# Performance work log

Measured on AMD Instinct MI355X. Metric: run time of the kernel, lower is better.

The kernel has to match this reference:

```python
import jax, jax.numpy as jnp
import numpy as np

B, T, Hs, Ws, D, NH, NKV = 2, 8, 16, 16, 1024, 16, 4
HD = D // NH  # 64
EPS = 1e-6
THETA = 10000.0


def setup_inputs() -> dict:
    key = jax.random.key(0)
    ks = jax.random.split(key, 6)
    N = T * Hs * Ws
    s = 0.02
    return {
        'x': jax.random.normal(ks[0], (B, N, D), jnp.float32),
        'Wq': jax.random.normal(ks[1], (D, D), jnp.float32) * s,
        'bq': jnp.zeros((D,), jnp.float32),
        'Wk': jax.random.normal(ks[2], (D, NKV * HD), jnp.float32) * s,
        'bk': jnp.zeros((NKV * HD,), jnp.float32),
        'Wv': jax.random.normal(ks[3], (D, NKV * HD), jnp.float32) * s,
        'bv': jnp.zeros((NKV * HD,), jnp.float32),
        'Wo': jax.random.normal(ks[4], (D, D), jnp.float32) * s,
        'bo': jnp.zeros((D,), jnp.float32),
        'qn_w': jnp.ones((HD,), jnp.float32),
        'kn_w': jnp.ones((HD,), jnp.float32),
        't': T, 'h': Hs, 'w': Ws,
    }


def _rms_norm(x, w):
    # RMSNorm over last dim (head_dim), eps=1e-6, learned scale
    var = jnp.mean(jnp.square(x), axis=-1, keepdims=True)
    return x * jax.lax.rsqrt(var + EPS) * w


def _rope_cs(n, d):
    inv = 1.0 / (THETA ** (np.arange(0, d, 2, dtype=np.float32) / d))
    fr = np.arange(n, dtype=np.float32)[:, None] * inv[None, :]
    emb = np.concatenate([fr, fr], axis=-1)  # (n, d)
    return jnp.asarray(np.cos(emb)), jnp.asarray(np.sin(emb))


def _rot_half(x):
    x1, x2 = jnp.split(x, 2, axis=-1)
    return jnp.concatenate([-x2, x1], axis=-1)


def _st_rope(x, t, h, w):
    # x: (B, t, h, w, heads, hd); factored 3D RoPE on head_dim split
    d = x.shape[-1]
    if d % 3 == 0:
        dt = dh = d // 3
        dw = d - 2 * dt
    else:
        dt = d // 4
        dh = d // 4
        dw = d - dt - dh
    xt, xh, xw = jnp.split(x, [dt, dt + dh], axis=-1)

    def app(xs, n, axis_pos, dd):
        cos, sin = _rope_cs(n, dd)
        shp = [1] * 6
        shp[axis_pos] = n
        shp[-1] = dd
        cos = cos.reshape(shp)
        sin = sin.reshape(shp)
        return xs * cos + _rot_half(xs) * sin

    xt = app(xt, t, 1, dt)
    xh = app(xh, h, 2, dh)
    xw = app(xw, w, 3, dw)
    return jnp.concatenate([xt, xh, xw], axis=-1)


def reference(x, Wq, bq, Wk, bk, Wv, bv, Wo, bo, qn_w, kn_w, t, h, w):
    Bx, N, Dx = x.shape
    q = (x @ Wq + bq).reshape(Bx, N, NH, HD)
    k = (x @ Wk + bk).reshape(Bx, N, NKV, HD)
    v = (x @ Wv + bv).reshape(Bx, N, NKV, HD)
    q = _rms_norm(q, qn_w)
    k = _rms_norm(k, kn_w)
    q = _st_rope(q.reshape(Bx, t, h, w, NH, HD), t, h, w).reshape(Bx, N, NH, HD)
    k = _st_rope(k.reshape(Bx, t, h, w, NKV, HD), t, h, w).reshape(Bx, N, NKV, HD)
    g = NH // NKV
    if g > 1:  # GQA: 'b m h d -> b m (h g) d'
        k = jnp.repeat(k, g, axis=2)
        v = jnp.repeat(v, g, axis=2)
    scale = HD ** -0.5
    scores = jnp.einsum('bnhd,bmhd->bhnm', q, k) * scale  # (B,H,N,N)
    p = jax.nn.softmax(scores, axis=-1)
    out = jnp.einsum('bhnm,bmhd->bnhd', p, v).reshape(Bx, N, Dx)
    return out @ Wo + bo
```

## Files before the change

kernel.cpp:

```cpp
#include <hip/hip_runtime.h>
#include <hip/hip_bf16.h>
#include <math.h>

constexpr int B_   = 2;
constexpr int N_   = 2048;
constexpr int D_   = 1024;
constexpr int NH_  = 16;
constexpr int NKV_ = 4;
constexpr int HD_  = 64;
constexpr int BN_  = 4096;
constexpr int KVD_ = NKV_ * HD_;
constexpr float EPS_ = 1e-6f;
constexpr float THETA_ = 10000.0f;
constexpr float LOG2E_ = 1.4426950408889634f;

typedef _Float16 half8v __attribute__((ext_vector_type(8)));
typedef _Float16 half4v __attribute__((ext_vector_type(4)));
typedef unsigned short ushort8v __attribute__((ext_vector_type(8)));
typedef float f32x4 __attribute__((ext_vector_type(4)));

static __device__ __forceinline__ unsigned short f2h(float f) {
  union { _Float16 h; unsigned short u; } v; v.h = (_Float16)f; return v.u;
}
static __device__ __forceinline__ float h2f(unsigned short u) {
  union { unsigned short u; _Float16 h; } v; v.u = u; return (float)v.h;
}

#if __has_builtin(__builtin_amdgcn_exp2f)
#define EXP2F(x) __builtin_amdgcn_exp2f(x)
#else
#define EXP2F(x) __expf((x) * 0.6931471805599453f)
#endif

static __device__ __forceinline__ void dma16(const unsigned short* g,
                                             unsigned short* l) {
  __builtin_amdgcn_global_load_lds(
      (const __attribute__((address_space(1))) unsigned int*)g,
      (__attribute__((address_space(3))) unsigned int*)l, 16, 0, 0);
}

static __device__ __forceinline__ void wtrans_tile(
    const float* __restrict__ W, int Nw, int K, float scale,
    unsigned short* __restrict__ WTh, unsigned short* __restrict__ WTl,
    int bx, int by, bool lo)
{
  __shared__ float tile[32][33];
  const int k0 = bx * 32, n0 = by * 32;
  const int c = threadIdx.x & 31, rb = threadIdx.x >> 5;
#pragma unroll
  for (int i = 0; i < 4; ++i) {
    const int r = rb + i * 8;
    tile[r][c] = W[(size_t)(k0 + r) * Nw + n0 + c];
  }
  __syncthreads();
#pragma unroll
  for (int i = 0; i < 4; ++i) {
    const int r = rb + i * 8;
    const float v = tile[c][r] * scale;
    const size_t o = (size_t)(n0 + r) * K + k0 + c;
    const unsigned short hi = f2h(v);
    WTh[o] = hi;
    if (lo) WTl[o] = f2h(v - h2f(hi));
  }
}

__global__ __launch_bounds__(256) void prep(
    const float* __restrict__ x,
    const float* __restrict__ Wq, const float* __restrict__ Wk,
    const float* __restrict__ Wv, const float* __restrict__ Wo,
    unsigned short* __restrict__ xh,
    unsigned short* __restrict__ WqT, unsigned short* __restrict__ WkT,
    unsigned short* __restrict__ WvT,
    unsigned short* __restrict__ WoT)
{
  const int bid = blockIdx.x;
  if (bid < 2048) {
    const int i = (bid * 256 + threadIdx.x) * 8;
    const float4 v0 = *(const float4*)(x + i);
    const float4 v1 = *(const float4*)(x + i + 4);
    ushort8v o;
    o[0] = f2h(v0.x); o[1] = f2h(v0.y); o[2] = f2h(v0.z); o[3] = f2h(v0.w);
    o[4] = f2h(v1.x); o[5] = f2h(v1.y); o[6] = f2h(v1.z); o[7] = f2h(v1.w);
    *(ushort8v*)(xh + i) = o;
  } else if (bid < 3072) {
    const int l = bid - 2048;
    wtrans_tile(Wq, D_, D_, 1.0f, WqT, nullptr, l & 31, l >> 5, false);
  } else if (bid < 3328) {
    const int l = bid - 3072;
    wtrans_tile(Wk, KVD_, D_, 1.0f, WkT, nullptr, l & 31, l >> 5, false);
  } else if (bid < 3584) {
    const int l = bid - 3328;
    wtrans_tile(Wv, KVD_, D_, 1.0f, WvT, nullptr, l & 31, l >> 5, false);
  } else {
    const int l = bid - 3584;
    wtrans_tile(Wo, D_, D_, 1.0f, WoT, nullptr, l & 31, l >> 5, false);
  }
}

__global__ __launch_bounds__(256) void gemm_qkv(
    const unsigned short* __restrict__ xh,
    const unsigned short* __restrict__ WqT, const unsigned short* __restrict__ WkT,
    const unsigned short* __restrict__ WvT,
    const float* __restrict__ bq, const float* __restrict__ bk, const float* __restrict__ bv,
    const float* __restrict__ qn, const float* __restrict__ kn,
    unsigned short* __restrict__ qv, unsigned short* __restrict__ kv,
    unsigned short* __restrict__ vv)
{
  __shared__ unsigned short As[2][128 * 64];
  __shared__ unsigned short Bs[2][64 * 64];

  const int bid = blockIdx.x;
  const int xcd = bid & 7;
  const int g   = bid >> 3;
  const int bx  = xcd * 4 + (g & 3);
  const int y   = g >> 2;

  const unsigned short* wt; const float* bias; unsigned short* outp; int opitch, col0, mode;
  if (y < 16)      { wt = WqT + (size_t)y * 64 * D_;        bias = bq + y * 64;        outp = qv; opitch = D_;   col0 = y * 64;        mode = 0; }
  else if (y < 20) { wt = WkT + (size_t)(y - 16) * 64 * D_; bias = bk + (y - 16) * 64; outp = kv; opitch = KVD_; col0 = (y - 16) * 64; mode = 1; }
  else             { wt = WvT + (size_t)(y - 20) * 64 * D_; bias = bv + (y - 20) * 64; outp = vv; opitch = KVD_; col0 = (y - 20) * 64; mode = 2; }

  const int bm = bx * 128;
  const int tid = threadIdx.x;
  const int w = tid >> 6, lane = tid & 63, quad = lane >> 4, l16 = lane & 15;
  const int lr = lane >> 3;
  const int gc = (lane & 7) ^ lr;
  const int sw = l16 & 7;

  const unsigned short* gA = xh + (size_t)(bm + w * 8 + lr) * D_ + gc * 8;
  const unsigned short* gB = wt + (size_t)(w * 8 + lr) * D_ + gc * 8;

  f32x4 acc[2][4];
#pragma unroll
  for (int i = 0; i < 2; ++i)
#pragma unroll
    for (int j = 0; j < 4; ++j) acc[i][j] = (f32x4){0.f, 0.f, 0.f, 0.f};

  for (int k0 = 0; k0 < D_; k0 += 128) {
    __syncthreads();
#pragma unroll
    for (int p = 0; p < 2; ++p) {
#pragma unroll
      for (int rd = 0; rd < 4; ++rd)
        dma16(gA + (size_t)rd * 32 * D_ + k0 + p * 64, &As[p][rd * 2048 + w * 512]);
#pragma unroll
      for (int rd = 0; rd < 2; ++rd)
        dma16(gB + (size_t)rd * 32 * D_ + k0 + p * 64, &Bs[p][rd * 2048 + w * 512]);
    }
    __syncthreads();

#pragma unroll
    for (int kk = 0; kk < 4; ++kk) {
      const int p = kk >> 1;
      const int slot = ((((kk & 1) * 4 + quad)) ^ sw) * 8;
      half8v fa[2], fb[4];
#pragma unroll
      for (int mb = 0; mb < 2; ++mb)
        fa[mb] = *(const half8v*)&As[p][(w * 32 + mb * 16 + l16) * 64 + slot];
#pragma unroll
      for (int nb = 0; nb < 4; ++nb)
        fb[nb] = *(const half8v*)&Bs[p][(nb * 16 + l16) * 64 + slot];
#pragma unroll
      for (int mb = 0; mb < 2; ++mb)
#pragma unroll
        for (int nb = 0; nb < 4; ++nb)
          acc[mb][nb] = __builtin_amdgcn_mfma_f32_16x16x32_f16(fa[mb], fb[nb], acc[mb][nb], 0, 0, 0);
    }
  }

  float bsv[4];
#pragma unroll
  for (int nb = 0; nb < 4; ++nb) bsv[nb] = bias[nb * 16 + l16];

  if (mode == 2) {
#pragma unroll
    for (int mb = 0; mb < 2; ++mb)
#pragma unroll
      for (int nb = 0; nb < 4; ++nb)
#pragma unroll
        for (int r = 0; r < 4; ++r) {
          const int row = bm + w * 32 + mb * 16 + quad * 4 + r;
          outp[(size_t)row * opitch + col0 + nb * 16 + l16] = f2h(acc[mb][nb][r] + bsv[nb]);
        }
    return;
  }

  const float* nwp = (mode == 0) ? qn : kn;
  float wv[4];
#pragma unroll
  for (int nb = 0; nb < 4; ++nb) wv[nb] = nwp[nb * 16 + l16];
  const float f_th = __powf(THETA_, -(float)(l16 & 7) / 8.0f);
  const float f_w  = __powf(THETA_, -(float)l16 / 16.0f);
  const float oscale = (mode == 0) ? 0.125f * LOG2E_ : 1.0f;
  const bool first8 = (l16 & 8) == 0;

  float snw[4], csw[4];
#pragma unroll
  for (int r = 0; r < 4; ++r)
    __sincosf((float)(quad * 4 + r) * f_w, &snw[r], &csw[r]);

#pragma unroll
  for (int mb = 0; mb < 2; ++mb) {
    const int nbase = (bm + w * 32 + mb * 16) & (N_ - 1);
    float snt, cst, snh, csh;
    __sincosf((float)(nbase >> 8) * f_th, &snt, &cst);
    __sincosf((float)((nbase >> 4) & 15) * f_th, &snh, &csh);
#pragma unroll
    for (int r = 0; r < 4; ++r) {
      float v[4];
      float ss = 0.f;
#pragma unroll
      for (int nb = 0; nb < 4; ++nb) { v[nb] = acc[mb][nb][r] + bsv[nb]; ss += v[nb] * v[nb]; }
      ss += __shfl_xor(ss, 1, 64);
      ss += __shfl_xor(ss, 2, 64);
      ss += __shfl_xor(ss, 4, 64);
      ss += __shfl_xor(ss, 8, 64);
      const float rs = rsqrtf(ss * (1.0f / 64.0f) + EPS_);
#pragma unroll
      for (int nb = 0; nb < 4; ++nb) v[nb] *= rs * wv[nb];

      const float p0 = __shfl_xor(v[0], 8, 64);
      const float p1 = __shfl_xor(v[1], 8, 64);
      const float o0 = v[0] * cst + (first8 ? -p0 : p0) * snt;
      const float o1 = v[1] * csh + (first8 ? -p1 : p1) * snh;
      const float o2 = v[2] * csw[r] - v[3] * snw[r];
      const float o3 = v[3] * csw[r] + v[2] * snw[r];

      const int row = bm + w * 32 + mb * 16 + quad * 4 + r;
      const size_t ob = (size_t)row * opitch + col0 + l16;
      outp[ob]      = f2h(o0 * oscale);
      outp[ob + 16] = f2h(o1 * oscale);
      outp[ob + 32] = f2h(o2 * oscale);
      outp[ob + 48] = f2h(o3 * oscale);
    }
  }
}

__global__ __launch_bounds__(256) void gemm_o(
    const unsigned short* __restrict__ ag,
    const unsigned short* __restrict__ WT,
    const float* __restrict__ bo, float* __restrict__ out)
{
  __shared__ unsigned short As[2][128 * 64];
  __shared__ unsigned short Bs[2][64 * 64];

  const int bid = blockIdx.x;
  const int xcd = bid & 7;
  const int g   = bid >> 3;
  const int bx  = xcd * 4 + (g & 3);
  const int by  = g >> 2;

  const int bm = bx * 128, bn = by * 64;
  const int tid = threadIdx.x;
  const int w = tid >> 6, lane = tid & 63, quad = lane >> 4, l16 = lane & 15;
  const int lr = lane >> 3;
  const int gc = (lane & 7) ^ lr;
  const int sw = l16 & 7;

  const unsigned short* gA = ag + (size_t)(bm + w * 8 + lr) * D_ + gc * 8;
  const unsigned short* gB = WT + (size_t)(bn + w * 8 + lr) * D_ + gc * 8;

  f32x4 acc[2][4];
#pragma unroll
  for (int i = 0; i < 2; ++i)
#pragma unroll
    for (int j = 0; j < 4; ++j) acc[i][j] = (f32x4){0.f, 0.f, 0.f, 0.f};

  for (int k0 = 0; k0 < D_; k0 += 128) {
    __syncthreads();
#pragma unroll
    for (int p = 0; p < 2; ++p) {
#pragma unroll
      for (int rd = 0; rd < 4; ++rd)
        dma16(gA + (size_t)rd * 32 * D_ + k0 + p * 64, &As[p][rd * 2048 + w * 512]);
#pragma unroll
      for (int rd = 0; rd < 2; ++rd)
        dma16(gB + (size_t)rd * 32 * D_ + k0 + p * 64, &Bs[p][rd * 2048 + w * 512]);
    }
    __syncthreads();

#pragma unroll
    for (int kk = 0; kk < 4; ++kk) {
      const int p = kk >> 1;
      const int slot = ((((kk & 1) * 4 + quad)) ^ sw) * 8;
      half8v fa[2], fb[4];
#pragma unroll
      for (int mb = 0; mb < 2; ++mb)
        fa[mb] = *(const half8v*)&As[p][(w * 32 + mb * 16 + l16) * 64 + slot];
#pragma unroll
      for (int nb = 0; nb < 4; ++nb)
        fb[nb] = *(const half8v*)&Bs[p][(nb * 16 + l16) * 64 + slot];
#pragma unroll
      for (int mb = 0; mb < 2; ++mb)
#pragma unroll
        for (int nb = 0; nb < 4; ++nb)
          acc[mb][nb] = __builtin_amdgcn_mfma_f32_16x16x32_f16(fa[mb], fb[nb], acc[mb][nb], 0, 0, 0);
    }
  }

  float bsv[4];
#pragma unroll
  for (int nb = 0; nb < 4; ++nb) bsv[nb] = bo[bn + nb * 16 + l16];
#pragma unroll
  for (int mb = 0; mb < 2; ++mb)
#pragma unroll
    for (int nb = 0; nb < 4; ++nb)
#pragma unroll
      for (int r = 0; r < 4; ++r) {
        const int row = bm + w * 32 + mb * 16 + quad * 4 + r;
        const int col = bn + nb * 16 + l16;
        out[(size_t)row * D_ + col] = acc[mb][nb][r] + bsv[nb];
      }
}

__global__ __launch_bounds__(512, 2) void attn_mfma(
    const unsigned short* __restrict__ qg,
    const unsigned short* __restrict__ kg,
    const unsigned short* __restrict__ vg,
    unsigned short* __restrict__ og)
{
  __shared__ unsigned short Ks[2][128 * 64];
  __shared__ unsigned short Vt[2][64][136];

  const int bid = blockIdx.x;
  const int xcd = bid & 7;
  const int g   = bid >> 3;
  const int b   = xcd >> 2;
  const int kvh = xcd & 3;
  const int h   = kvh * 4 + (g & 3);
  const int qt  = g >> 2;

  const int tid  = threadIdx.x;
  const int w    = tid >> 6;
  const int lane = tid & 63;
  const int quad = lane >> 4;
  const int l16  = lane & 15;
  const int lr = lane >> 3;
  const int gc = (lane & 7) ^ lr;
  const int sw = l16 & 7;

  half8v aq[2][2];
#pragma unroll
  for (int qb = 0; qb < 2; ++qb) {
    const int qrow = qt * 256 + w * 32 + qb * 16 + l16;
    const unsigned short* qptr =
        qg + ((size_t)(b * N_ + qrow) * D_) + h * HD_ + quad * 8;
    aq[qb][0] = *(const half8v*)(qptr);
    aq[qb][1] = *(const half8v*)(qptr + 32);
  }

  f32x4 o_[2][4];
  float lrow[2] = {0.f, 0.f};
#pragma unroll
  for (int qb = 0; qb < 2; ++qb)
#pragma unroll
    for (int i = 0; i < 4; ++i) o_[qb][i] = (f32x4){0.f, 0.f, 0.f, 0.f};

  const unsigned short* gK =
      kg + ((size_t)(b * N_) + w * 8 + lr) * KVD_ + kvh * HD_ + gc * 8;

  const int vj  = tid & 15;
  const int vh  = (tid >> 4) & 1;
  const int vs  = (tid >> 5) & 7;
  const int vhh = tid >> 8;
  const int vcol = vhh * 64 + vh * 32 +
                   ((vj >> 1) & 3) * 8 + ((vj >> 3) & 1) * 4 + 2 * (vj & 1);
  const unsigned short* gV =
      vg + (size_t)(b * N_ + vhh * 64 + 2 * vj + 32 * vh) * KVD_ + kvh * HD_ + 8 * vs;

#pragma unroll
  for (int rd = 0; rd < 2; ++rd)
    dma16(gK + (size_t)(rd * 64) * KVD_, &Ks[0][rd * 4096 + w * 512]);
  ushort8v va0 = *(const ushort8v*)(gV);
  ushort8v va1 = *(const ushort8v*)(gV + KVD_);
#pragma unroll
  for (int i = 0; i < 8; ++i)
    *(unsigned int*)&Vt[0][8 * vs + i][vcol] =
        (unsigned int)va0[i] | ((unsigned int)va1[i] << 16);
  {
    const unsigned short* p = gV + (size_t)128 * KVD_;
    va0 = *(const ushort8v*)(p);
    va1 = *(const ushort8v*)(p + KVD_);
  }
  __syncthreads();

  for (int kt = 0; kt < 16; ++kt) {
    const int cur = kt & 1;
    if (kt < 15) {
#pragma unroll
      for (int rd = 0; rd < 2; ++rd)
        dma16(gK + (size_t)((kt + 1) * 128 + rd * 64) * KVD_,
              &Ks[cur ^ 1][rd * 4096 + w * 512]);
#pragma unroll
      for (int i = 0; i < 8; ++i)
        *(unsigned int*)&Vt[cur ^ 1][8 * vs + i][vcol] =
            (unsigned int)va0[i] | ((unsigned int)va1[i] << 16);
      if (kt < 14) {
        const unsigned short* p = gV + (size_t)(kt + 2) * 128 * KVD_;
        va0 = *(const ushort8v*)(p);
        va1 = *(const ushort8v*)(p + KVD_);
      }
    }

#pragma unroll
    for (int hh = 0; hh < 2; ++hh) {
      f32x4 s[2][4];
#pragma unroll
      for (int nb = 0; nb < 4; ++nb) {
        const int kr = (hh * 64 + nb * 16 + l16) * 64;
        const half8v b0 = *(const half8v*)&Ks[cur][kr + (quad ^ sw) * 8];
        const half8v b1 = *(const half8v*)&Ks[cur][kr + ((4 + quad) ^ sw) * 8];
#pragma unroll
        for (int qb = 0; qb < 2; ++qb) {
          f32x4 z = (f32x4){0.f, 0.f, 0.f, 0.f};
          z = __builtin_amdgcn_mfma_f32_16x16x32_f16(b0, aq[qb][0], z, 0, 0, 0);
          s[qb][nb] = __builtin_amdgcn_mfma_f32_16x16x32_f16(b1, aq[qb][1], z, 0, 0, 0);
        }
      }

      half8v pf[2][2];
#pragma unroll
      for (int qb = 0; qb < 2; ++qb) {
        float ls = 0.f;
#pragma unroll
        for (int nb = 0; nb < 4; ++nb) {
          const float p0 = EXP2F(s[qb][nb][0]);
          const float p1 = EXP2F(s[qb][nb][1]);
          const float p2 = EXP2F(s[qb][nb][2]);
          const float p3 = EXP2F(s[qb][nb][3]);
          ls += (p0 + p1) + (p2 + p3);
          const int kc = nb >> 1, jo = (nb & 1) * 4;
          pf[qb][kc][jo + 0] = (_Float16)p0;
          pf[qb][kc][jo + 1] = (_Float16)p1;
          pf[qb][kc][jo + 2] = (_Float16)p2;
          pf[qb][kc][jo + 3] = (_Float16)p3;
        }
        lrow[qb] += ls;
      }

#pragma unroll
      for (int kc = 0; kc < 2; ++kc)
#pragma unroll
        for (int nb = 0; nb < 4; ++nb) {
          const half8v bv =
              *(const half8v*)&Vt[cur][nb * 16 + l16][hh * 64 + kc * 32 + quad * 8];
#pragma unroll
          for (int qb = 0; qb < 2; ++qb)
            o_[qb][nb] = __builtin_amdgcn_mfma_f32_16x16x32_f16(bv, pf[qb][kc], o_[qb][nb], 0, 0, 0);
        }
    }
    __syncthreads();
  }

#pragma unroll
  for (int qb = 0; qb < 2; ++qb) {
    float l = lrow[qb];
    l += __shfl_xor(l, 16, 64);
    l += __shfl_xor(l, 32, 64);
    const float inv = 1.0f / l;
    const int qrow = qt * 256 + w * 32 + qb * 16 + l16;
    const size_t base = (size_t)(b * N_ + qrow) * D_ + h * HD_;
#pragma unroll
    for (int nb = 0; nb < 4; ++nb) {
      half4v pk;
#pragma unroll
      for (int r = 0; r < 4; ++r) pk[r] = (_Float16)(o_[qb][nb][r] * inv);
      *(half4v*)&og[base + nb * 16 + quad * 4] = pk;
    }
  }
}

extern "C" void kernel_launch(void* const* d_in, const int* in_sizes, int n_in,
                              void* d_out, int out_size, void* d_ws, size_t ws_size,
                              hipStream_t stream) {
  const float* x  = (const float*)d_in[0];
  const float* Wq = (const float*)d_in[1];
  const float* bq = (const float*)d_in[2];
  const float* Wk = (const float*)d_in[3];
  const float* bk = (const float*)d_in[4];
  const float* Wv = (const float*)d_in[5];
  const float* bv = (const float*)d_in[6];
  const float* Wo = (const float*)d_in[7];
  const float* bo = (const float*)d_in[8];
  const float* qn = (const float*)d_in[9];
  const float* kn = (const float*)d_in[10];
  float* out = (float*)d_out;

  const size_t M4 = (size_t)BN_ * D_;
  const size_t M1 = (size_t)BN_ * KVD_;
  unsigned short* xh  = (unsigned short*)d_ws;
  unsigned short* qv  = xh + M4;
  unsigned short* kv  = qv + M4;
  unsigned short* vv  = kv + M1;
  unsigned short* WqT = vv + M1;
  unsigned short* WkT = WqT + (size_t)D_ * D_;
  unsigned short* WvT = WkT + (size_t)D_ * KVD_;
  unsigned short* WoT = WvT + (size_t)D_ * KVD_;
  unsigned short* og  = xh;

  const dim3 blk(256);

  prep<<<dim3(4608), blk, 0, stream>>>(x, Wq, Wk, Wv, Wo, xh, WqT, WkT, WvT, WoT);

  gemm_qkv<<<dim3(768), blk, 0, stream>>>(xh, WqT, WkT, WvT, bq, bk, bv, qn, kn, qv, kv, vv);

  attn_mfma<<<dim3(256), dim3(512), 0, stream>>>(qv, kv, vv, og);

  gemm_o<<<dim3(512), blk, 0, stream>>>(og, WoT, bo, out);
}
```

Baseline: 173.2 us.

## Split attention over two key halves and merge partials in a combine kernel

Each attention block now handles only half of the key/value sequence, which doubles the grid from 256 to 512 blocks so every CU can host two blocks under its launch bounds. Each block writes an fp16 partial output plus its row-sum to workspace. A new combine kernel weights the two partials by their normalisers to produce the final attention output. This trades better CU occupancy and latency hiding for extra workspace traffic and one more kernel launch.

```diff
diff --git a/kernel.cpp b/kernel.cpp
--- a/kernel.cpp
+++ b/kernel.cpp
@@ -317,7 +317,8 @@
     const unsigned short* __restrict__ qg,
     const unsigned short* __restrict__ kg,
     const unsigned short* __restrict__ vg,
-    unsigned short* __restrict__ og)
+    unsigned short* __restrict__ po,
+    float* __restrict__ pl)
 {
   __shared__ unsigned short Ks[2][128 * 64];
   __shared__ unsigned short Vt[2][64][136];
@@ -327,8 +328,9 @@
   const int g   = bid >> 3;
   const int b   = xcd >> 2;
   const int kvh = xcd & 3;
+  const int ks  = g >> 5;
+  const int qt  = (g >> 2) & 7;
   const int h   = kvh * 4 + (g & 3);
-  const int qt  = g >> 2;
 
   const int tid  = threadIdx.x;
   const int w    = tid >> 6;
@@ -357,7 +359,7 @@
     for (int i = 0; i < 4; ++i) o_[qb][i] = (f32x4){0.f, 0.f, 0.f, 0.f};
 
   const unsigned short* gK =
-      kg + ((size_t)(b * N_) + w * 8 + lr) * KVD_ + kvh * HD_ + gc * 8;
+      kg + ((size_t)(b * N_ + ks * 1024) + w * 8 + lr) * KVD_ + kvh * HD_ + gc * 8;
 
   const int vj  = tid & 15;
   const int vh  = (tid >> 4) & 1;
@@ -366,7 +368,7 @@
   const int vcol = vhh * 64 + vh * 32 +
                    ((vj >> 1) & 3) * 8 + ((vj >> 3) & 1) * 4 + 2 * (vj & 1);
   const unsigned short* gV =
-      vg + (size_t)(b * N_ + vhh * 64 + 2 * vj + 32 * vh) * KVD_ + kvh * HD_ + 8 * vs;
+      vg + (size_t)(b * N_ + ks * 1024 + vhh * 64 + 2 * vj + 32 * vh) * KVD_ + kvh * HD_ + 8 * vs;
 
 #pragma unroll
   for (int rd = 0; rd < 2; ++rd)
@@ -384,9 +386,9 @@
   }
   __syncthreads();
 
-  for (int kt = 0; kt < 16; ++kt) {
+  for (int kt = 0; kt < 8; ++kt) {
     const int cur = kt & 1;
-    if (kt < 15) {
+    if (kt < 7) {
 #pragma unroll
       for (int rd = 0; rd < 2; ++rd)
         dma16(gK + (size_t)((kt + 1) * 128 + rd * 64) * KVD_,
@@ -395,7 +397,7 @@
       for (int i = 0; i < 8; ++i)
         *(unsigned int*)&Vt[cur ^ 1][8 * vs + i][vcol] =
             (unsigned int)va0[i] | ((unsigned int)va1[i] << 16);
-      if (kt < 14) {
+      if (kt < 6) {
         const unsigned short* p = gV + (size_t)(kt + 2) * 128 * KVD_;
         va0 = *(const ushort8v*)(p);
         va1 = *(const ushort8v*)(p + KVD_);
@@ -459,15 +461,38 @@
     l += __shfl_xor(l, 32, 64);
     const float inv = 1.0f / l;
     const int qrow = qt * 256 + w * 32 + qb * 16 + l16;
-    const size_t base = (size_t)(b * N_ + qrow) * D_ + h * HD_;
+    const size_t rowg = (size_t)(b * N_ + qrow);
+    if (quad == 0) pl[((size_t)ks * 4096 + rowg) * 16 + h] = l;
+    const size_t base = ((size_t)ks * 4096 + rowg) * D_ + h * HD_;
 #pragma unroll
     for (int nb = 0; nb < 4; ++nb) {
       half4v pk;
 #pragma unroll
       for (int r = 0; r < 4; ++r) pk[r] = (_Float16)(o_[qb][nb][r] * inv);
-      *(half4v*)&og[base + nb * 16 + quad * 4] = pk;
-    }
-  }
+      *(half4v*)&po[base + nb * 16 + quad * 4] = pk;
+    }
+  }
+}
+
+__global__ __launch_bounds__(256) void combine(
+    const unsigned short* __restrict__ po, const float* __restrict__ pl,
+    unsigned short* __restrict__ og)
+{
+  const int idx = blockIdx.x * 256 + threadIdx.x;
+  const int e = idx * 8;
+  const int row = e >> 10;
+  const int h = (e >> 6) & 15;
+  const float l0 = pl[(size_t)row * 16 + h];
+  const float l1 = pl[(size_t)(4096 + row) * 16 + h];
+  const float inv = 1.0f / (l0 + l1);
+  const float w0 = l0 * inv, w1 = l1 * inv;
+  const ushort8v a = *(const ushort8v*)(po + e);
+  const ushort8v c = *(const ushort8v*)(po + (size_t)4096 * 1024 + e);
+  ushort8v o;
+#pragma unroll
+  for (int i = 0; i < 8; ++i)
+    o[i] = f2h(h2f(a[i]) * w0 + h2f(c[i]) * w1);
+  *(ushort8v*)(og + e) = o;
 }
 
 extern "C" void kernel_launch(void* const* d_in, const int* in_sizes, int n_in,
@@ -496,6 +521,8 @@
   unsigned short* WkT = WqT + (size_t)D_ * D_;
   unsigned short* WvT = WkT + (size_t)D_ * KVD_;
   unsigned short* WoT = WvT + (size_t)D_ * KVD_;
+  unsigned short* pov = WoT + (size_t)D_ * D_;
+  float* plv = (float*)(pov + (size_t)2 * 4096 * 1024);
   unsigned short* og  = xh;
 
   const dim3 blk(256);
@@ -504,7 +531,9 @@
 
   gemm_qkv<<<dim3(768), blk, 0, stream>>>(xh, WqT, WkT, WvT, bq, bk, bv, qn, kn, qv, kv, vv);
 
-  attn_mfma<<<dim3(256), dim3(512), 0, stream>>>(qv, kv, vv, og);
+  attn_mfma<<<dim3(512), dim3(512), 0, stream>>>(qv, kv, vv, pov, plv);
+
+  combine<<<dim3(2048), blk, 0, stream>>>(pov, plv, og);
 
   gemm_o<<<dim3(512), blk, 0, stream>>>(og, WoT, bo, out);
 }
```

Measured after the change: 179.8 us. 1.04x slower.
